# Performance work log

Measured on AMD Instinct MI355X. Metric: run time of the kernel, lower is better.

The kernel has to match this reference:

```python
import jax, jax.numpy as jnp
import numpy as np
import math

D_MODEL = 1024
NUM_HEADS = 16
B, L = 2, 2048
# scale_level=0, patch_time_span=1 -> effective_stride=1
PERIODS = (1.0, 30.0)
WEIGHTS = (0.8, 0.4)
SIGMAS = (0.5, 2.0)


def setup_inputs() -> dict:
    key = jax.random.key(0)
    ks = jax.random.split(key, 10)
    s = 1.0 / math.sqrt(D_MODEL)
    inp = {
        "x": jax.random.normal(ks[0], (B, L, D_MODEL), dtype=jnp.float32),
        "Wq": jax.random.normal(ks[1], (D_MODEL, D_MODEL), dtype=jnp.float32) * s,
        "bq": jax.random.normal(ks[2], (D_MODEL,), dtype=jnp.float32) * 0.01,
        "Wk": jax.random.normal(ks[3], (D_MODEL, D_MODEL), dtype=jnp.float32) * s,
        "bk": jax.random.normal(ks[4], (D_MODEL,), dtype=jnp.float32) * 0.01,
        "Wv": jax.random.normal(ks[5], (D_MODEL, D_MODEL), dtype=jnp.float32) * s,
        "bv": jax.random.normal(ks[6], (D_MODEL,), dtype=jnp.float32) * 0.01,
        "Wo": jax.random.normal(ks[7], (D_MODEL, D_MODEL), dtype=jnp.float32) * s,
        "bo": jax.random.normal(ks[8], (D_MODEL,), dtype=jnp.float32) * 0.01,
        "prior_lambda": jnp.asarray(2.0, dtype=jnp.float32),
    }
    return inp


def _gaussian_mask(length):
    idx = jnp.arange(length, dtype=jnp.float32)
    delta = jnp.abs(idx[:, None] - idx[None, :])  # [L, L]
    mask = jnp.zeros_like(delta)
    for p, w, sigma in zip(PERIODS, WEIGHTS, SIGMAS):
        if p < 0.2:
            continue
        mask = mask + w * jnp.exp(-((delta - p) ** 2) / (2.0 * sigma ** 2))
    return mask


def reference(x, Wq, bq, Wk, bk, Wv, bv, Wo, bo, prior_lambda):
    Bx, Lx, D = x.shape
    H = NUM_HEADS
    hd = D // H

    def split_heads(t):  # [B, L, D] -> [B, H, L, hd]
        return t.reshape(Bx, Lx, H, hd).transpose(0, 2, 1, 3)

    Q = split_heads(x @ Wq.T + bq)
    K = split_heads(x @ Wk.T + bk)
    V = split_heads(x @ Wv.T + bv)

    scores = jnp.einsum("bhqd,bhkd->bhqk", Q, K) / math.sqrt(hd)
    scores = scores + prior_lambda * _gaussian_mask(Lx)[None, None, :, :]
    attn = jax.nn.softmax(scores, axis=-1)
    out = jnp.einsum("bhqk,bhkd->bhqd", attn, V)
    out = out.transpose(0, 2, 1, 3).reshape(Bx, Lx, D)
    return out @ Wo.T + bo
```

## Files before the change

kernel.cpp:

```cpp
#include <hip/hip_runtime.h>

#define D_MODEL 1024
#define SEQ_L   2048
#define NHEADS  16
#define HDIM    64
#define NROWS   4096

#define QSCALE 0.18033688011112042f
#define LOG2E  1.4426950408889634f

#if __has_builtin(__builtin_amdgcn_exp2f)
#define EXP2F(x) __builtin_amdgcn_exp2f(x)
#else
#define EXP2F(x) __expf((x) * 0.6931471805599453f)
#endif

typedef __attribute__((ext_vector_type(8))) short short8;
typedef __attribute__((ext_vector_type(4))) short short4v;
typedef __attribute__((ext_vector_type(4))) float floatx4;
typedef __attribute__((ext_vector_type(4))) unsigned short ushort4v;
typedef unsigned short ushort;

static __device__ __forceinline__ ushort f2bf(float f) {
    unsigned int u = __float_as_uint(f);
    u += 0x7FFFu + ((u >> 16) & 1u);
    return (ushort)(u >> 16);
}

static __device__ __forceinline__ floatx4 mfma16(short8 a, short8 b, floatx4 c) {
    return __builtin_amdgcn_mfma_f32_16x16x32_bf16(a, b, c, 0, 0, 0);
}

static __device__ __forceinline__ void store8bf(ushort* dst, float4 a, float4 b) {
    uint4 pk;
    pk.x = (unsigned)f2bf(a.x) | ((unsigned)f2bf(a.y) << 16);
    pk.y = (unsigned)f2bf(a.z) | ((unsigned)f2bf(a.w) << 16);
    pk.z = (unsigned)f2bf(b.x) | ((unsigned)f2bf(b.y) << 16);
    pk.w = (unsigned)f2bf(b.z) | ((unsigned)f2bf(b.w) << 16);
    *(uint4*)dst = pk;
}

static __device__ __forceinline__ void gll16(const ushort* g, ushort* l) {
    __builtin_amdgcn_global_load_lds(
        (const __attribute__((address_space(1))) unsigned int*)(const unsigned int*)g,
        (__attribute__((address_space(3))) unsigned int*)(unsigned int*)l,
        16, 0, 0);
}

__global__ __launch_bounds__(256) void convert_bf16(
    const float* __restrict__ x,
    const float* __restrict__ wq, const float* __restrict__ wk,
    const float* __restrict__ wv, const float* __restrict__ wo,
    ushort* __restrict__ xb, ushort* __restrict__ wb3, ushort* __restrict__ wob)
{
    const int seg = blockIdx.y;
    const float* src;
    ushort* dst;
    int n;
    if      (seg == 0) { src = x;  dst = xb;                n = 4194304; }
    else if (seg == 1) { src = wq; dst = wb3;               n = 1048576; }
    else if (seg == 2) { src = wk; dst = wb3 + 1048576;     n = 1048576; }
    else if (seg == 3) { src = wv; dst = wb3 + 2097152;     n = 1048576; }
    else               { src = wo; dst = wob;               n = 1048576; }
    const int i = (blockIdx.x * 256 + threadIdx.x) * 8;
    if (i >= n) return;
    float4 a = *(const float4*)(src + i);
    float4 b = *(const float4*)(src + i + 4);
    store8bf(dst + i, a, b);
}

__global__ __launch_bounds__(256, 4) void gemm_qkv(
    const ushort* __restrict__ A, const ushort* __restrict__ B,
    const float* __restrict__ bq, const float* __restrict__ bk,
    const float* __restrict__ bv,
    ushort* __restrict__ Qo, ushort* __restrict__ Ko, ushort* __restrict__ Vo)
{
    __shared__ ushort As[64 * 64];
    __shared__ ushort Bs[128 * 64];

    const int tid  = threadIdx.x;
    const int w    = tid >> 6;
    const int lane = tid & 63;
    const int l15  = lane & 15;
    const int quad = lane >> 4;

    const int bm = blockIdx.y * 64;
    const int bn = blockIdx.x * 128;
    const int z  = blockIdx.x >> 3;

    const int ciA0 = tid,        ciA1 = tid + 256;
    const int rA0 = ciA0 >> 3,   rA1 = ciA1 >> 3;
    const int sA0i = ciA0 & 7,   sA1i = ciA1 & 7;
    const ushort* aP0 = A + (size_t)(bm + rA0) * 1024 + (sA0i ^ (rA0 & 7)) * 8;
    const ushort* aP1 = A + (size_t)(bm + rA1) * 1024 + (sA1i ^ (rA1 & 7)) * 8;
    ushort* lA0 = &As[rA0 * 64 + sA0i * 8];
    ushort* lA1 = &As[rA1 * 64 + sA1i * 8];

    const ushort* bP[4];
    ushort* lB[4];
#pragma unroll
    for (int p = 0; p < 4; p++) {
        const int ci = tid + p * 256;
        const int r = ci >> 3, s = ci & 7;
        bP[p] = B + (size_t)(bn + r) * 1024 + (s ^ (r & 7)) * 8;
        lB[p] = &Bs[r * 64 + s * 8];
    }

    const int x7 = l15 & 7;

    floatx4 acc[4][2];
#pragma unroll
    for (int i = 0; i < 4; i++)
#pragma unroll
        for (int j = 0; j < 2; j++) acc[i][j] = (floatx4){0.f, 0.f, 0.f, 0.f};

    for (int k0 = 0; k0 < 1024; k0 += 64) {
        __syncthreads();
        gll16(aP0 + k0, lA0);
        gll16(aP1 + k0, lA1);
#pragma unroll
        for (int p = 0; p < 4; p++) gll16(bP[p] + k0, lB[p]);
        __syncthreads();

#pragma unroll
        for (int kk = 0; kk < 2; kk++) {
            const int slot = ((kk * 4 + quad) ^ x7) * 8;
            short8 af[4], bf[2];
#pragma unroll
            for (int mi = 0; mi < 4; mi++)
                af[mi] = *(const short8*)&As[(mi * 16 + l15) * 64 + slot];
#pragma unroll
            for (int ni = 0; ni < 2; ni++)
                bf[ni] = *(const short8*)&Bs[(w * 32 + ni * 16 + l15) * 64 + slot];
            if (z == 2) {
#pragma unroll
                for (int mi = 0; mi < 4; mi++)
#pragma unroll
                    for (int ni = 0; ni < 2; ni++)
                        acc[mi][ni] = mfma16(af[mi], bf[ni], acc[mi][ni]);
            } else {
#pragma unroll
                for (int mi = 0; mi < 4; mi++)
#pragma unroll
                    for (int ni = 0; ni < 2; ni++)
                        acc[mi][ni] = mfma16(bf[ni], af[mi], acc[mi][ni]);
            }
        }
    }

    __syncthreads();
    ushort* St = Bs;
    const int cwbase = bn & 1023;
    const int bb = bm >> 11;

    if (z == 2) {
#pragma unroll
        for (int ni = 0; ni < 2; ni++) {
            const int hdp = w * 32 + ni * 16 + l15;
            const float bvl = bv[cwbase + hdp];
            const int xr = (hdp & 7) << 1;
#pragma unroll
            for (int mi = 0; mi < 4; mi++) {
                ushort4v pk;
#pragma unroll
                for (int r = 0; r < 4; r++) pk[r] = f2bf(acc[mi][ni][r] + bvl);
                const int gs = (mi * 4 + quad) ^ xr;
                *(ushort4v*)&St[hdp * 64 + gs * 4] = pk;
            }
        }
        __syncthreads();
        const int li0 = bm & 2047;
        const int c = lane & 7;
#pragma unroll
        for (int t = 0; t < 4; t++) {
            const int hdp = w * 32 + t * 8 + (lane >> 3);
            const int h  = (cwbase >> 6) + (hdp >> 6);
            const int hd = hdp & 63;
            const int gs = (2 * c) ^ ((hdp & 7) << 1);
            uint4 vdat = *(const uint4*)&St[hdp * 64 + gs * 4];
            *(uint4*)(Vo + ((size_t)(bb * NHEADS + h) * HDIM + hd) * SEQ_L + li0 + c * 8) = vdat;
        }
    } else {
        const float* bias = z ? bk : bq;
        const float scale = z ? 1.0f : QSCALE;
        ushort* outp = z ? Ko : Qo;
#pragma unroll
        for (int ni = 0; ni < 2; ni++) {
            const int colw = cwbase + w * 32 + ni * 16 + quad * 4;
            const float4 bb4 = *(const float4*)&bias[colw];
#pragma unroll
            for (int mi = 0; mi < 4; mi++) {
                const int row = mi * 16 + l15;
                ushort4v pk;
                pk[0] = f2bf((acc[mi][ni][0] + bb4.x) * scale);
                pk[1] = f2bf((acc[mi][ni][1] + bb4.y) * scale);
                pk[2] = f2bf((acc[mi][ni][2] + bb4.z) * scale);
                pk[3] = f2bf((acc[mi][ni][3] + bb4.w) * scale);
                const int gs = (w * 8 + ni * 4 + quad) ^ ((row & 7) << 2);
                *(ushort4v*)&St[row * 128 + gs * 4] = pk;
            }
        }
        __syncthreads();
        const int c = l15;
        const int h0 = cwbase >> 6;
        const int h  = h0 + (c >> 3);
        const int hd0 = (c & 7) * 8;
#pragma unroll
        for (int t = 0; t < 4; t++) {
            const int row = w * 16 + t * 4 + quad;
            const int li = (bm + row) & 2047;
            const int gs = (2 * c) ^ ((row & 7) << 2);
            uint4 vdat = *(const uint4*)&St[row * 128 + gs * 4];
            *(uint4*)(outp + ((size_t)(bb * NHEADS + h) * SEQ_L + li) * HDIM + hd0) = vdat;
        }
    }
}

__global__ __launch_bounds__(512, 4) void attn(
    const ushort* __restrict__ Q,
    const ushort* __restrict__ K,
    const ushort* __restrict__ Vt,
    const float* __restrict__ lam,
    ushort* __restrict__ Aout)
{
    __shared__ float mtab[128];
    __shared__ ushort Ks[2][64 * 64];
    __shared__ ushort Vts[2][64 * 64];

    const int tid  = threadIdx.x;
    const int wave = tid >> 6;
    const int lane = tid & 63;
    const int l15  = lane & 15;
    const int quad = lane >> 4;

    const int qb = blockIdx.x;
    const int h  = blockIdx.y;
    const int bz = blockIdx.z;
    const int bh = bz * NHEADS + h;
    const int q0 = qb * 128;

    const float lambda = *lam;
    if (tid < 128) {
        float d  = (float)tid;
        float e1 = (d - 1.f) * (d - 1.f);
        float e2 = (d - 30.f) * (d - 30.f);
        mtab[tid] = LOG2E * lambda *
                    (0.8f * __expf(-2.0f * e1) + 0.4f * __expf(-0.125f * e2));
    }

    const int qg = q0 + wave * 16 + l15;
    const ushort* qp = Q + ((size_t)bh * SEQ_L + qg) * HDIM + quad * 8;
    short8 qf[2];
    qf[0] = *(const short8*)qp;
    qf[1] = *(const short8*)(qp + 32);

    const ushort* kbase = K  + ((size_t)bh * SEQ_L) * HDIM;
    const ushort* vbase = Vt + ((size_t)bh * HDIM) * SEQ_L;

    const int cid = tid;
    const int rowc = cid >> 3;
    const int clc  = (cid & 7) ^ (rowc & 7);
    const ushort* kg = kbase + (size_t)rowc * HDIM + clc * 8;
    const ushort* vg = vbase + (size_t)rowc * SEQ_L + clc * 8;

    floatx4 o[4];
#pragma unroll
    for (int i = 0; i < 4; i++) o[i] = (floatx4){0.f, 0.f, 0.f, 0.f};
    floatx4 ol = (floatx4){0.f, 0.f, 0.f, 0.f};

    uint4 onesw;
    onesw.x = 0x3F803F80u; onesw.y = 0x3F803F80u;
    onesw.z = 0x3F803F80u; onesw.w = 0x3F803F80u;
    const short8 ones8 = __builtin_bit_cast(short8, onesw);

    gll16(kg, &Ks[0][cid * 8]);
    gll16(vg, &Vts[0][cid * 8]);

    const int xo = l15 & 7;
    const int g64 = wave >> 2;

    for (int t = 0; t < 32; t++) {
        const int cur = t & 1;
        __syncthreads();
        if (t + 1 < 32) {
            const int nxt = cur ^ 1;
            const int koff = (t + 1) * 64;
            gll16(kg + (size_t)koff * HDIM, &Ks[nxt][cid * 8]);
            gll16(vg + koff, &Vts[nxt][cid * 8]);
        }

        floatx4 s[4];
#pragma unroll
        for (int i = 0; i < 4; i++) s[i] = (floatx4){0.f, 0.f, 0.f, 0.f};
#pragma unroll
        for (int kk = 0; kk < 2; kk++) {
#pragma unroll
            for (int nt = 0; nt < 4; nt++) {
                const int slot = (kk * 4 + quad) ^ xo;
                short8 kf = *(const short8*)&Ks[cur][(nt * 16 + l15) * 64 + slot * 8];
                s[nt] = mfma16(kf, qf[kk], s[nt]);
            }
        }

        const int tg = t - (qb * 2 + g64);
        if (tg >= -1 && tg <= 1) {
#pragma unroll
            for (int nt = 0; nt < 4; nt++) {
                const int kgi = t * 64 + nt * 16 + quad * 4;
#pragma unroll
                for (int r = 0; r < 4; r++) {
                    int dq = qg - (kgi + r);
                    int ad = dq < 0 ? -dq : dq;
                    s[nt][r] += mtab[ad];
                }
            }
        }

        short8 pb8[2];
#pragma unroll
        for (int c = 0; c < 2; c++) {
            unsigned ur[8];
#pragma unroll
            for (int r = 0; r < 4; r++)
                ur[r] = __float_as_uint(EXP2F(s[2 * c][r])) + 0x8000u;
#pragma unroll
            for (int r = 0; r < 4; r++)
                ur[4 + r] = __float_as_uint(EXP2F(s[2 * c + 1][r])) + 0x8000u;
            uint4 pk;
            pk.x = __builtin_amdgcn_perm(ur[1], ur[0], 0x07060302u);
            pk.y = __builtin_amdgcn_perm(ur[3], ur[2], 0x07060302u);
            pk.z = __builtin_amdgcn_perm(ur[5], ur[4], 0x07060302u);
            pk.w = __builtin_amdgcn_perm(ur[7], ur[6], 0x07060302u);
            pb8[c] = __builtin_bit_cast(short8, pk);
        }

#pragma unroll
        for (int c = 0; c < 2; c++) {
#pragma unroll
            for (int nt = 0; nt < 4; nt++) {
                const int glo = ((c << 2) + (quad >> 1)) ^ xo;
                const int ghi = glo ^ 2;
                const int rb  = (nt * 16 + l15) * 64 + (quad & 1) * 4;
                short4v vlo = *(const short4v*)&Vts[cur][rb + glo * 8];
                short4v vhi = *(const short4v*)&Vts[cur][rb + ghi * 8];
                short8 vf8 = __builtin_shufflevector(vlo, vhi, 0, 1, 2, 3, 4, 5, 6, 7);
                o[nt] = mfma16(vf8, pb8[c], o[nt]);
            }
            ol = mfma16(ones8, pb8[c], ol);
        }
    }

    const float linv = 1.0f / ol[0];
    ushort* obase = Aout + ((size_t)bz * SEQ_L + qg) * D_MODEL + h * HDIM;
#pragma unroll
    for (int nt = 0; nt < 4; nt++) {
        ushort4v pk;
#pragma unroll
        for (int r = 0; r < 4; r++) pk[r] = f2bf(o[nt][r] * linv);
        *(ushort4v*)(obase + nt * 16 + quad * 4) = pk;
    }
}

__global__ __launch_bounds__(256, 4) void gemm_out(
    const ushort* __restrict__ A, const ushort* __restrict__ B,
    const float* __restrict__ bo, float* __restrict__ out)
{
    __shared__ ushort As[64 * 64];
    __shared__ ushort Bs[64 * 64];

    const int tid  = threadIdx.x;
    const int w    = tid >> 6;
    const int lane = tid & 63;
    const int l15  = lane & 15;
    const int quad = lane >> 4;

    const int bm = blockIdx.y * 64;
    const int bn = blockIdx.x * 64;

    const int ci0 = tid, ci1 = tid + 256;
    const int r0 = ci0 >> 3, r1 = ci1 >> 3;
    const int s0 = ci0 & 7,  s1 = ci1 & 7;
    const ushort* aP0 = A + (size_t)(bm + r0) * 1024 + (s0 ^ (r0 & 7)) * 8;
    const ushort* aP1 = A + (size_t)(bm + r1) * 1024 + (s1 ^ (r1 & 7)) * 8;
    const ushort* bP0 = B + (size_t)(bn + r0) * 1024 + (s0 ^ (r0 & 7)) * 8;
    const ushort* bP1 = B + (size_t)(bn + r1) * 1024 + (s1 ^ (r1 & 7)) * 8;
    ushort* lA0 = &As[r0 * 64 + s0 * 8];
    ushort* lA1 = &As[r1 * 64 + s1 * 8];
    ushort* lB0 = &Bs[r0 * 64 + s0 * 8];
    ushort* lB1 = &Bs[r1 * 64 + s1 * 8];

    const int x7 = l15 & 7;

    floatx4 acc[4];
#pragma unroll
    for (int i = 0; i < 4; i++) acc[i] = (floatx4){0.f, 0.f, 0.f, 0.f};

    for (int k0 = 0; k0 < 1024; k0 += 64) {
        __syncthreads();
        gll16(aP0 + k0, lA0);
        gll16(aP1 + k0, lA1);
        gll16(bP0 + k0, lB0);
        gll16(bP1 + k0, lB1);
        __syncthreads();

#pragma unroll
        for (int kk = 0; kk < 2; kk++) {
            const int slot = ((kk * 4 + quad) ^ x7) * 8;
            short8 bf = *(const short8*)&Bs[(w * 16 + l15) * 64 + slot];
#pragma unroll
            for (int mi = 0; mi < 4; mi++) {
                short8 af = *(const short8*)&As[(mi * 16 + l15) * 64 + slot];
                acc[mi] = mfma16(bf, af, acc[mi]);
            }
        }
    }

    const int col0 = bn + w * 16 + quad * 4;
    const float4 bb4 = *(const float4*)&bo[col0];
#pragma unroll
    for (int mi = 0; mi < 4; mi++) {
        const int row = bm + mi * 16 + l15;
        float4 st;
        st.x = acc[mi][0] + bb4.x;
        st.y = acc[mi][1] + bb4.y;
        st.z = acc[mi][2] + bb4.z;
        st.w = acc[mi][3] + bb4.w;
        *(float4*)(out + (size_t)row * 1024 + col0) = st;
    }
}

extern "C" void kernel_launch(void* const* d_in, const int* in_sizes, int n_in,
                              void* d_out, int out_size, void* d_ws, size_t ws_size,
                              hipStream_t stream)
{
    const float* x   = (const float*)d_in[0];
    const float* Wq  = (const float*)d_in[1];
    const float* bq  = (const float*)d_in[2];
    const float* Wk  = (const float*)d_in[3];
    const float* bk  = (const float*)d_in[4];
    const float* Wv  = (const float*)d_in[5];
    const float* bv  = (const float*)d_in[6];
    const float* Wo  = (const float*)d_in[7];
    const float* bo  = (const float*)d_in[8];
    const float* lam = (const float*)d_in[9];
    float* out = (float*)d_out;

    const size_t NELEM = (size_t)NROWS * D_MODEL;
    ushort* Qw  = (ushort*)d_ws;
    ushort* Kw  = Qw + NELEM;
    ushort* Vw  = Kw + NELEM;
    ushort* XA  = Vw + NELEM;
    ushort* Wb3 = XA + NELEM;
    ushort* Wob = Wb3 + 3 * 1024 * 1024;

    dim3 gc(2048, 5);
    convert_bf16<<<gc, 256, 0, stream>>>(x, Wq, Wk, Wv, Wo, XA, Wb3, Wob);

    dim3 g1(3072 / 128, NROWS / 64);
    gemm_qkv<<<g1, 256, 0, stream>>>(XA, Wb3, bq, bk, bv, Qw, Kw, Vw);

    dim3 g2(SEQ_L / 128, NHEADS, 2);
    attn<<<g2, 512, 0, stream>>>(Qw, Kw, Vw, lam, XA);

    dim3 g3(1024 / 64, NROWS / 64);
    gemm_out<<<g3, 256, 0, stream>>>(XA, Wob, bo, out);
}
```

Measured before the change: 195.5 us.

## Split attention key tile across wave pairs with shared-memory output reduction

Each wave now handles two 16-row query groups but only half of each 64-key tile, so every K fragment loaded from LDS feeds two MFMAs and each V fragment read serves two query groups. The partial O and row-sum accumulators from the two key halves are combined through shared memory after the loop, reusing the K/V buffers as scratch. This halves per-wave LDS fragment traffic per MFMA, at the cost of more accumulator registers, an extra reduction phase with two barriers, and half the waves going idle during the epilogue.

Measured after the change: 197.7 us. No clear change (+1.1%).

```diff
diff --git a/kernel.cpp b/kernel.cpp
--- a/kernel.cpp
+++ b/kernel.cpp
@@ -226,9 +226,12 @@
     __shared__ float mtab[128];
     __shared__ ushort Ks[2][64 * 64];
     __shared__ ushort Vts[2][64 * 64];
+    __shared__ float olred[512];
 
     const int tid  = threadIdx.x;
     const int wave = tid >> 6;
+    const int ws   = wave & 3;
+    const int ks   = wave >> 2;
     const int lane = tid & 63;
     const int l15  = lane & 15;
     const int quad = lane >> 4;
@@ -248,11 +251,13 @@
                     (0.8f * __expf(-2.0f * e1) + 0.4f * __expf(-0.125f * e2));
     }
 
-    const int qg = q0 + wave * 16 + l15;
-    const ushort* qp = Q + ((size_t)bh * SEQ_L + qg) * HDIM + quad * 8;
-    short8 qf[2];
-    qf[0] = *(const short8*)qp;
-    qf[1] = *(const short8*)(qp + 32);
+    const ushort* qp =
+        Q + ((size_t)bh * SEQ_L + q0 + ws * 16 + l15) * HDIM + quad * 8;
+    short8 qf[2][2];
+    qf[0][0] = *(const short8*)qp;
+    qf[0][1] = *(const short8*)(qp + 32);
+    qf[1][0] = *(const short8*)(qp + 64 * HDIM);
+    qf[1][1] = *(const short8*)(qp + 64 * HDIM + 32);
 
     const ushort* kbase = K  + ((size_t)bh * SEQ_L) * HDIM;
     const ushort* vbase = Vt + ((size_t)bh * HDIM) * SEQ_L;
@@ -263,10 +268,14 @@
     const ushort* kg = kbase + (size_t)rowc * HDIM + clc * 8;
     const ushort* vg = vbase + (size_t)rowc * SEQ_L + clc * 8;
 
-    floatx4 o[4];
-#pragma unroll
-    for (int i = 0; i < 4; i++) o[i] = (floatx4){0.f, 0.f, 0.f, 0.f};
-    floatx4 ol = (floatx4){0.f, 0.f, 0.f, 0.f};
+    floatx4 o[2][4];
+#pragma unroll
+    for (int g = 0; g < 2; g++)
+#pragma unroll
+        for (int i = 0; i < 4; i++) o[g][i] = (floatx4){0.f, 0.f, 0.f, 0.f};
+    floatx4 ol[2];
+    ol[0] = (floatx4){0.f, 0.f, 0.f, 0.f};
+    ol[1] = (floatx4){0.f, 0.f, 0.f, 0.f};
 
     uint4 onesw;
     onesw.x = 0x3F803F80u; onesw.y = 0x3F803F80u;
@@ -276,8 +285,8 @@
     gll16(kg, &Ks[0][cid * 8]);
     gll16(vg, &Vts[0][cid * 8]);
 
-    const int xo = l15 & 7;
-    const int g64 = wave >> 2;
+    const int xo  = l15 & 7;
+    const int nt0 = ks * 2;
 
     for (int t = 0; t < 32; t++) {
         const int cur = t & 1;
@@ -289,75 +298,103 @@
             gll16(vg + koff, &Vts[nxt][cid * 8]);
         }
 
-        floatx4 s[4];
-#pragma unroll
-        for (int i = 0; i < 4; i++) s[i] = (floatx4){0.f, 0.f, 0.f, 0.f};
+        floatx4 s[2][2];
+#pragma unroll
+        for (int g = 0; g < 2; g++)
+#pragma unroll
+            for (int j = 0; j < 2; j++) s[g][j] = (floatx4){0.f, 0.f, 0.f, 0.f};
 #pragma unroll
         for (int kk = 0; kk < 2; kk++) {
-#pragma unroll
-            for (int nt = 0; nt < 4; nt++) {
-                const int slot = (kk * 4 + quad) ^ xo;
+            const int slot = (kk * 4 + quad) ^ xo;
+#pragma unroll
+            for (int j = 0; j < 2; j++) {
+                const int nt = nt0 + j;
                 short8 kf = *(const short8*)&Ks[cur][(nt * 16 + l15) * 64 + slot * 8];
-                s[nt] = mfma16(kf, qf[kk], s[nt]);
-            }
-        }
-
-        const int tg = t - (qb * 2 + g64);
-        if (tg >= -1 && tg <= 1) {
-#pragma unroll
-            for (int nt = 0; nt < 4; nt++) {
-                const int kgi = t * 64 + nt * 16 + quad * 4;
-#pragma unroll
-                for (int r = 0; r < 4; r++) {
-                    int dq = qg - (kgi + r);
-                    int ad = dq < 0 ? -dq : dq;
-                    s[nt][r] += mtab[ad];
+                s[0][j] = mfma16(kf, qf[0][kk], s[0][j]);
+                s[1][j] = mfma16(kf, qf[1][kk], s[1][j]);
+            }
+        }
+
+#pragma unroll
+        for (int g = 0; g < 2; g++) {
+            const int tg = t - (qb * 2 + g);
+            if (tg >= -1 && tg <= 1) {
+                const int qg = q0 + g * 64 + ws * 16 + l15;
+#pragma unroll
+                for (int j = 0; j < 2; j++) {
+                    const int kgi = t * 64 + (nt0 + j) * 16 + quad * 4;
+#pragma unroll
+                    for (int r = 0; r < 4; r++) {
+                        int dq = qg - (kgi + r);
+                        int ad = dq < 0 ? -dq : dq;
+                        s[g][j][r] += mtab[ad];
+                    }
                 }
             }
         }
 
         short8 pb8[2];
 #pragma unroll
-        for (int c = 0; c < 2; c++) {
+        for (int g = 0; g < 2; g++) {
             unsigned ur[8];
 #pragma unroll
             for (int r = 0; r < 4; r++)
-                ur[r] = __float_as_uint(EXP2F(s[2 * c][r])) + 0x8000u;
+                ur[r] = __float_as_uint(EXP2F(s[g][0][r])) + 0x8000u;
 #pragma unroll
             for (int r = 0; r < 4; r++)
-                ur[4 + r] = __float_as_uint(EXP2F(s[2 * c + 1][r])) + 0x8000u;
+                ur[4 + r] = __float_as_uint(EXP2F(s[g][1][r])) + 0x8000u;
             uint4 pk;
             pk.x = __builtin_amdgcn_perm(ur[1], ur[0], 0x07060302u);
             pk.y = __builtin_amdgcn_perm(ur[3], ur[2], 0x07060302u);
             pk.z = __builtin_amdgcn_perm(ur[5], ur[4], 0x07060302u);
             pk.w = __builtin_amdgcn_perm(ur[7], ur[6], 0x07060302u);
-            pb8[c] = __builtin_bit_cast(short8, pk);
-        }
-
-#pragma unroll
-        for (int c = 0; c < 2; c++) {
+            pb8[g] = __builtin_bit_cast(short8, pk);
+        }
+
+        const int glo = ((ks << 2) + (quad >> 1)) ^ xo;
+        const int ghi = glo ^ 2;
+#pragma unroll
+        for (int nt = 0; nt < 4; nt++) {
+            const int rb = (nt * 16 + l15) * 64 + (quad & 1) * 4;
+            short4v vlo = *(const short4v*)&Vts[cur][rb + glo * 8];
+            short4v vhi = *(const short4v*)&Vts[cur][rb + ghi * 8];
+            short8 vf8 = __builtin_shufflevector(vlo, vhi, 0, 1, 2, 3, 4, 5, 6, 7);
+            o[0][nt] = mfma16(vf8, pb8[0], o[0][nt]);
+            o[1][nt] = mfma16(vf8, pb8[1], o[1][nt]);
+        }
+        ol[0] = mfma16(ones8, pb8[0], ol[0]);
+        ol[1] = mfma16(ones8, pb8[1], ol[1]);
+    }
+
+    __syncthreads();
+    float* redb = (ws < 2) ? (float*)&Ks[0][0] : (float*)&Vts[0][0];
+    const int wsl = ws & 1;
+    if (ks == 1) {
+#pragma unroll
+        for (int g = 0; g < 2; g++) {
+#pragma unroll
+            for (int nt = 0; nt < 4; nt++)
+                *(floatx4*)&redb[wsl * 2048 + ((g * 4 + nt) * 64 + lane) * 4] = o[g][nt];
+            olred[((ws * 2 + g) * 64) + lane] = ol[g][0];
+        }
+    }
+    __syncthreads();
+    if (ks == 0) {
+#pragma unroll
+        for (int g = 0; g < 2; g++) {
+            const float l = ol[g][0] + olred[((ws * 2 + g) * 64) + lane];
+            const float linv = 1.0f / l;
+            const int qg = q0 + g * 64 + ws * 16 + l15;
+            ushort* obase = Aout + ((size_t)bz * SEQ_L + qg) * D_MODEL + h * HDIM;
 #pragma unroll
             for (int nt = 0; nt < 4; nt++) {
-                const int glo = ((c << 2) + (quad >> 1)) ^ xo;
-                const int ghi = glo ^ 2;
-                const int rb  = (nt * 16 + l15) * 64 + (quad & 1) * 4;
-                short4v vlo = *(const short4v*)&Vts[cur][rb + glo * 8];
-                short4v vhi = *(const short4v*)&Vts[cur][rb + ghi * 8];
-                short8 vf8 = __builtin_shufflevector(vlo, vhi, 0, 1, 2, 3, 4, 5, 6, 7);
-                o[nt] = mfma16(vf8, pb8[c], o[nt]);
-            }
-            ol = mfma16(ones8, pb8[c], ol);
-        }
-    }
-
-    const float linv = 1.0f / ol[0];
-    ushort* obase = Aout + ((size_t)bz * SEQ_L + qg) * D_MODEL + h * HDIM;
-#pragma unroll
-    for (int nt = 0; nt < 4; nt++) {
-        ushort4v pk;
-#pragma unroll
-        for (int r = 0; r < 4; r++) pk[r] = f2bf(o[nt][r] * linv);
-        *(ushort4v*)(obase + nt * 16 + quad * 4) = pk;
+                floatx4 op = *(const floatx4*)&redb[wsl * 2048 + ((g * 4 + nt) * 64 + lane) * 4];
+                ushort4v pk;
+#pragma unroll
+                for (int r = 0; r < 4; r++) pk[r] = f2bf((o[g][nt][r] + op[r]) * linv);
+                *(ushort4v*)(obase + nt * 16 + quad * 4) = pk;
+            }
+        }
     }
 }
 
```
